# Performance work log

Hardware: AMD Instinct MI355X
Metric: run time of the kernel (lower is better)

## Reference

```python
import jax, jax.numpy as jnp
import numpy as np

N_NODES = 50000
N_EDGES = 800000
D = 128


def gcn_conv(x, W, b, src, dst, num_nodes):
    """PyG GCNConv: x @ W, add self-loops, symmetric normalization, scatter-add, + bias."""
    x = x @ W  # [N, out]
    loop = jnp.arange(num_nodes, dtype=src.dtype)
    s = jnp.concatenate([src, loop])  # [E+N]
    d = jnp.concatenate([dst, loop])
    w = jnp.ones(s.shape[0], x.dtype)  # edge_weight=None -> ones (self-loop fill=1)
    deg = jax.ops.segment_sum(w, d, num_segments=num_nodes)  # [N]
    dinv = jnp.where(deg > 0, jax.lax.rsqrt(deg), 0.0)
    norm = dinv[s] * dinv[d]  # [E+N]
    out = jax.ops.segment_sum(x[s] * norm[:, None], d, num_segments=num_nodes)
    return out + b


def setup_inputs() -> dict:
    key = jax.random.key(0)
    ks = jax.random.split(key, 8)
    sc = 1.0 / np.sqrt(D)
    x = jax.random.normal(ks[0], (N_NODES, D), dtype=jnp.float32)
    edge_index = jax.random.randint(ks[1], (2, N_EDGES), 0, N_NODES)
    W1 = jax.random.normal(ks[2], (D, D), dtype=jnp.float32) * sc
    W2 = jax.random.normal(ks[3], (D, D), dtype=jnp.float32) * sc
    W3 = jax.random.normal(ks[4], (D, D), dtype=jnp.float32) * sc
    b1 = jnp.zeros((D,), jnp.float32)
    b2 = jnp.zeros((D,), jnp.float32)
    b3 = jnp.zeros((D,), jnp.float32)
    return {"x": x, "edge_index": edge_index, "W1": W1, "b1": b1,
            "W2": W2, "b2": b2, "W3": W3, "b3": b3}


def reference(x, edge_index, W1, b1, W2, b2, W3, b3):
    src, dst = edge_index[0], edge_index[1]
    n = x.shape[0]
    x = jax.nn.relu(gcn_conv(x, W1, b1, src, dst, n))
    x = jax.nn.relu(gcn_conv(x, W2, b2, src, dst, n))
    return gcn_conv(x, W3, b3, src, dst, n)
```

## Files before the change

kernel.cpp:

```cpp
#include <hip/hip_runtime.h>
#include <hip/hip_fp16.h>
#include <math.h>

#define D 128

typedef __attribute__((ext_vector_type(8))) _Float16 half8;
typedef __attribute__((ext_vector_type(4))) float f32x4;



__global__ void prep_kernel(const float* __restrict__ W1, const float* __restrict__ W2,
                            const float* __restrict__ W3, __half* __restrict__ WhT,
                            int* __restrict__ cnt, int N) {
    int i = blockIdx.x * blockDim.x + threadIdx.x;
    if (i < 3 * D * D) {
        int l = i >> 14;
        int j = i & 16383;
        int n = j >> 7, k = j & 127;
        const float* W = (l == 0) ? W1 : (l == 1) ? W2 : W3;
        WhT[(size_t)i] = __float2half(W[(size_t)k * D + n]);
    }
    if (i < N) cnt[i] = 0;
}


__global__ void count_rank_kernel(const int* __restrict__ dst, int* __restrict__ cnt,
                                  int* __restrict__ rank, int E) {
    int e0 = (blockIdx.x * blockDim.x + threadIdx.x) * 8;
    if (e0 + 7 < E) {
        int4 da = *(const int4*)(dst + e0);
        int4 db = *(const int4*)(dst + e0 + 4);
        int4 ra, rb;
        ra.x = atomicAdd(&cnt[da.x], 1);
        ra.y = atomicAdd(&cnt[da.y], 1);
        ra.z = atomicAdd(&cnt[da.z], 1);
        ra.w = atomicAdd(&cnt[da.w], 1);
        rb.x = atomicAdd(&cnt[db.x], 1);
        rb.y = atomicAdd(&cnt[db.y], 1);
        rb.z = atomicAdd(&cnt[db.z], 1);
        rb.w = atomicAdd(&cnt[db.w], 1);
        *(int4*)(rank + e0)     = ra;
        *(int4*)(rank + e0 + 4) = rb;
    } else {
        for (int e = e0; e < E; ++e) rank[e] = atomicAdd(&cnt[dst[e]], 1);
    }
}

__global__ __launch_bounds__(1024) void scan_kernel(const int* __restrict__ cnt,
                                                    int* __restrict__ rowptr,
                                                    float* __restrict__ dinv,
                                                    int N) {
    __shared__ int wsum[16];
    int tid  = threadIdx.x;
    int lane = tid & 63;
    int wid  = tid >> 6;
    int C = ((N + 4095) / 4096) * 4;
    int start = tid * C;
    int end   = start + C; if (end > N) end = N;

    int local = 0;
    int i = start;
    for (; i + 3 < end; i += 4) {
        int4 v = *(const int4*)(cnt + i);
        local += v.x + v.y + v.z + v.w;
    }
    for (; i < end; ++i) local += cnt[i];

    int sc = local;
    #pragma unroll
    for (int off = 1; off < 64; off <<= 1) {
        int t = __shfl_up(sc, off, 64);
        if (lane >= off) sc += t;
    }
    if (lane == 63) wsum[wid] = sc;
    __syncthreads();
    if (tid < 16) {
        int w = wsum[tid];
        #pragma unroll
        for (int off = 1; off < 16; off <<= 1) {
            int t = __shfl_up(w, off, 16);
            if (tid >= off) w += t;
        }
        wsum[tid] = w;
    }
    __syncthreads();
    int run = ((wid > 0) ? wsum[wid - 1] : 0) + (sc - local);

    i = start;
    for (; i + 3 < end; i += 4) {
        int4 v = *(const int4*)(cnt + i);
        int4 rp;
        rp.x = run;
        rp.y = rp.x + v.x;
        rp.z = rp.y + v.y;
        rp.w = rp.z + v.z;
        run  = rp.w + v.w;
        *(int4*)(rowptr + i) = rp;
        float4 dv;
        dv.x = rsqrtf((float)v.x + 1.0f);
        dv.y = rsqrtf((float)v.y + 1.0f);
        dv.z = rsqrtf((float)v.z + 1.0f);
        dv.w = rsqrtf((float)v.w + 1.0f);
        *(float4*)(dinv + i) = dv;
    }
    for (; i < end; ++i) {
        int v = cnt[i];
        rowptr[i] = run; run += v;
        dinv[i] = rsqrtf((float)v + 1.0f);
    }
    if (tid == 0) rowptr[N] = wsum[15];
}


__global__ __launch_bounds__(256) void fill_gemm1_kernel(
    const int* __restrict__ src, const int* __restrict__ dst,
    const int* __restrict__ rank, const int* __restrict__ rowptr,
    int* __restrict__ col, int E, int fill_blocks,
    const float* __restrict__ X, const __half* __restrict__ WhT,
    const float* __restrict__ dinv, __half* __restrict__ Y, int M) {
    int tid = threadIdx.x;
    if ((int)blockIdx.x < fill_blocks) {
        int e0 = (blockIdx.x * 256 + tid) * 8;
        if (e0 + 7 < E) {
            int4 da = *(const int4*)(dst + e0);
            int4 db = *(const int4*)(dst + e0 + 4);
            int4 ra = *(const int4*)(rank + e0);
            int4 rb = *(const int4*)(rank + e0 + 4);
            int4 sa = *(const int4*)(src + e0);
            int4 sb = *(const int4*)(src + e0 + 4);
            int p0 = rowptr[da.x] + ra.x;
            int p1 = rowptr[da.y] + ra.y;
            int p2 = rowptr[da.z] + ra.z;
            int p3 = rowptr[da.w] + ra.w;
            int p4 = rowptr[db.x] + rb.x;
            int p5 = rowptr[db.y] + rb.y;
            int p6 = rowptr[db.z] + rb.z;
            int p7 = rowptr[db.w] + rb.w;
            col[p0] = sa.x; col[p1] = sa.y; col[p2] = sa.z; col[p3] = sa.w;
            col[p4] = sb.x; col[p5] = sb.y; col[p6] = sb.z; col[p7] = sb.w;
        } else {
            for (int e = e0; e < E; ++e) col[rowptr[dst[e]] + rank[e]] = src[e];
        }
        return;
    }
    int bid  = blockIdx.x - fill_blocks;
    int wave = tid >> 6;
    int lane = tid & 63;
    int quad = lane >> 4;
    int l16  = lane & 15;
    int m0   = bid * 64 + wave * 16;
    if (m0 >= M) return;

    f32x4 acc[8];
    #pragma unroll
    for (int t = 0; t < 8; ++t) acc[t] = (f32x4)0.0f;

    const float* xrow = X + (size_t)(m0 + l16) * D;

    #pragma unroll
    for (int ks = 0; ks < 4; ++ks) {
        int k0 = ks * 32 + quad * 8;
        float4 x0 = *(const float4*)(xrow + k0);
        float4 x1 = *(const float4*)(xrow + k0 + 4);
        half8 a;
        a[0] = (_Float16)x0.x; a[1] = (_Float16)x0.y;
        a[2] = (_Float16)x0.z; a[3] = (_Float16)x0.w;
        a[4] = (_Float16)x1.x; a[5] = (_Float16)x1.y;
        a[6] = (_Float16)x1.z; a[7] = (_Float16)x1.w;
        #pragma unroll
        for (int t = 0; t < 8; ++t) {
            half8 b = *(const half8*)(WhT + (size_t)(t * 16 + l16) * D + k0);
            acc[t] = __builtin_amdgcn_mfma_f32_16x16x32_f16(a, b, acc[t], 0, 0, 0);
        }
    }

    float4 dv = *(const float4*)(dinv + m0 + quad * 4);
    float dvs[4] = {dv.x, dv.y, dv.z, dv.w};
    #pragma unroll
    for (int t = 0; t < 8; ++t) {
        #pragma unroll
        for (int r = 0; r < 4; ++r) {
            int grow = m0 + quad * 4 + r;
            Y[((size_t)t * M + grow) * 16 + l16] = __float2half(acc[t][r] * dvs[r]);
        }
    }
}


__global__ __launch_bounds__(256) void gemm_s_kernel(const __half* __restrict__ Xs,
                                                     const __half* __restrict__ WhT,
                                                     const float* __restrict__ dinv,
                                                     __half* __restrict__ Ys, int M) {
    int tid  = threadIdx.x;
    int wave = tid >> 6;
    int lane = tid & 63;
    int quad = lane >> 4;
    int l16  = lane & 15;
    int m0   = blockIdx.x * 64 + wave * 16;
    if (m0 >= M) return;

    f32x4 acc[8];
    #pragma unroll
    for (int t = 0; t < 8; ++t) acc[t] = (f32x4)0.0f;

    int arow = m0 + l16;

    #pragma unroll
    for (int ks = 0; ks < 4; ++ks) {
        int k0 = ks * 32 + quad * 8;
        half8 a = *(const half8*)(Xs + ((size_t)(k0 >> 4) * M + arow) * 16 + (k0 & 15));
        #pragma unroll
        for (int t = 0; t < 8; ++t) {
            half8 b = *(const half8*)(WhT + (size_t)(t * 16 + l16) * D + k0);
            acc[t] = __builtin_amdgcn_mfma_f32_16x16x32_f16(a, b, acc[t], 0, 0, 0);
        }
    }

    float4 dv = *(const float4*)(dinv + m0 + quad * 4);
    float dvs[4] = {dv.x, dv.y, dv.z, dv.w};
    #pragma unroll
    for (int t = 0; t < 8; ++t) {
        #pragma unroll
        for (int r = 0; r < 4; ++r) {
            int grow = m0 + quad * 4 + r;
            Ys[((size_t)t * M + grow) * 16 + l16] = __float2half(acc[t][r] * dvs[r]);
        }
    }
}


template <bool FINAL>
__global__ __launch_bounds__(256) void agg_slice_kernel(
    const __half* __restrict__ ysIn, const int* __restrict__ rowptr,
    const int* __restrict__ col, const float* __restrict__ dinv,
    const float* __restrict__ bias, __half* __restrict__ outh,
    float* __restrict__ outf, int M) {
    int bid   = blockIdx.x;
    int slice = bid & 7;
    int chunk = bid >> 3;
    int tid  = threadIdx.x;
    int wave = tid >> 6;
    int lane = tid & 63;
    int g    = lane >> 3;
    int l8   = lane & 7;
    int row  = chunk * 32 + wave * 8 + g;
    bool valid = row < M;
    int c = valid ? row : M - 1;

    const __half* base = ysIn + (size_t)slice * M * 16;
    int s = rowptr[c], e = rowptr[c + 1];

    float2 bb = ((const float2*)bias)[slice * 8 + l8];

    __half2 hself = *(const __half2*)(base + (size_t)c * 16 + l8 * 2);
    float a0x = __low2float(hself), a0y = __high2float(hself);
    float a1x = 0.f, a1y = 0.f, a2x = 0.f, a2y = 0.f, a3x = 0.f, a3y = 0.f;

    int j = s;
    for (; j + 8 <= e; j += 8) {
        int c0 = col[j + 0], c1 = col[j + 1], c2 = col[j + 2], c3 = col[j + 3];
        int c4 = col[j + 4], c5 = col[j + 5], c6 = col[j + 6], c7 = col[j + 7];
        __half2 v0 = *(const __half2*)(base + (size_t)c0 * 16 + l8 * 2);
        __half2 v1 = *(const __half2*)(base + (size_t)c1 * 16 + l8 * 2);
        __half2 v2 = *(const __half2*)(base + (size_t)c2 * 16 + l8 * 2);
        __half2 v3 = *(const __half2*)(base + (size_t)c3 * 16 + l8 * 2);
        __half2 v4 = *(const __half2*)(base + (size_t)c4 * 16 + l8 * 2);
        __half2 v5 = *(const __half2*)(base + (size_t)c5 * 16 + l8 * 2);
        __half2 v6 = *(const __half2*)(base + (size_t)c6 * 16 + l8 * 2);
        __half2 v7 = *(const __half2*)(base + (size_t)c7 * 16 + l8 * 2);
        a0x += __low2float(v0); a0y += __high2float(v0);
        a1x += __low2float(v1); a1y += __high2float(v1);
        a2x += __low2float(v2); a2y += __high2float(v2);
        a3x += __low2float(v3); a3y += __high2float(v3);
        a0x += __low2float(v4); a0y += __high2float(v4);
        a1x += __low2float(v5); a1y += __high2float(v5);
        a2x += __low2float(v6); a2y += __high2float(v6);
        a3x += __low2float(v7); a3y += __high2float(v7);
    }
    for (; j + 4 <= e; j += 4) {
        int c0 = col[j + 0], c1 = col[j + 1], c2 = col[j + 2], c3 = col[j + 3];
        __half2 v0 = *(const __half2*)(base + (size_t)c0 * 16 + l8 * 2);
        __half2 v1 = *(const __half2*)(base + (size_t)c1 * 16 + l8 * 2);
        __half2 v2 = *(const __half2*)(base + (size_t)c2 * 16 + l8 * 2);
        __half2 v3 = *(const __half2*)(base + (size_t)c3 * 16 + l8 * 2);
        a0x += __low2float(v0); a0y += __high2float(v0);
        a1x += __low2float(v1); a1y += __high2float(v1);
        a2x += __low2float(v2); a2y += __high2float(v2);
        a3x += __low2float(v3); a3y += __high2float(v3);
    }
    for (; j < e; ++j) {
        int c0 = col[j];
        __half2 v0 = *(const __half2*)(base + (size_t)c0 * 16 + l8 * 2);
        a0x += __low2float(v0); a0y += __high2float(v0);
    }
    a0x += a1x + a2x + a3x;
    a0y += a1y + a2y + a3y;

    float dv = dinv[c];
    float rx = bb.x + dv * a0x;
    float ry = bb.y + dv * a0y;
    if (valid) {
        if (FINAL) {
            *(float2*)(outf + (size_t)row * D + slice * 16 + l8 * 2) = make_float2(rx, ry);
        } else {
            __half2 hv = __floats2half2_rn(fmaxf(rx, 0.f), fmaxf(ry, 0.f));
            *(__half2*)(outh + ((size_t)slice * M + row) * 16 + l8 * 2) = hv;
        }
    }
}


extern "C" void kernel_launch(void* const* d_in, const int* in_sizes, int n_in,
                              void* d_out, int out_size, void* d_ws, size_t ws_size,
                              hipStream_t stream) {
    const float* x   = (const float*)d_in[0];
    const int*   ei  = (const int*)d_in[1];
    const float* W1  = (const float*)d_in[2];
    const float* b1  = (const float*)d_in[3];
    const float* W2  = (const float*)d_in[4];
    const float* b2  = (const float*)d_in[5];
    const float* W3  = (const float*)d_in[6];
    const float* b3  = (const float*)d_in[7];
    float* out = (float*)d_out;

    const int N = in_sizes[0] / D;
    const int E = in_sizes[1] / 2;
    const int* src = ei;
    const int* dst = ei + E;

    char* ws = (char*)d_ws;
    size_t off = 0;
    auto alloc = [&](size_t bytes) {
        void* p = ws + off;
        off = (off + bytes + 255) & ~(size_t)255;
        return p;
    };
    __half* ys    = (__half*)alloc((size_t)N * D * sizeof(__half));
    __half* hs    = (__half*)alloc((size_t)N * D * sizeof(__half));
    int*   cnt    = (int*)alloc((size_t)N * sizeof(int));
    int*   rowptr = (int*)alloc((size_t)(N + 1) * sizeof(int));
    float* dinv   = (float*)alloc((size_t)N * sizeof(float));
    int*   rank   = (int*)alloc((size_t)E * sizeof(int));
    int*   col    = (int*)alloc((size_t)E * sizeof(int));
    __half* WhT   = (__half*)alloc((size_t)3 * D * D * sizeof(__half));
    (void)ws_size; (void)n_in; (void)out_size;

    int prep_threads = (3 * D * D > N) ? 3 * D * D : N;
    prep_kernel<<<(prep_threads + 255) / 256, 256, 0, stream>>>(W1, W2, W3, WhT, cnt, N);

    const int egrid = ((E + 7) / 8 + 255) / 256;
    count_rank_kernel<<<egrid, 256, 0, stream>>>(dst, cnt, rank, E);
    scan_kernel<<<1, 1024, 0, stream>>>(cnt, rowptr, dinv, N);

    const int gemm_grid = (N + 63) / 64;
    fill_gemm1_kernel<<<egrid + gemm_grid, 256, 0, stream>>>(
        src, dst, rank, rowptr, col, E, egrid, x, WhT, dinv, ys, N);

    const int nchunk = (N + 31) / 32;
    const int agg_grid = nchunk * 8;
    agg_slice_kernel<false><<<agg_grid, 256, 0, stream>>>(ys, rowptr, col, dinv, b1, hs, nullptr, N);
    gemm_s_kernel<<<gemm_grid, 256, 0, stream>>>(hs, WhT + 16384, dinv, ys, N);
    agg_slice_kernel<false><<<agg_grid, 256, 0, stream>>>(ys, rowptr, col, dinv, b2, hs, nullptr, N);
    gemm_s_kernel<<<gemm_grid, 256, 0, stream>>>(hs, WhT + 32768, dinv, ys, N);
    agg_slice_kernel<true><<<agg_grid, 256, 0, stream>>>(ys, rowptr, col, dinv, b3, nullptr, out, N);
}
```

Before: 345.2 us.

## Widen feature slices from 16 to 32 halves for aggregation gathers

Changes the sliced intermediate feature layout from 8 slices of 16 halves to 4 slices of 32 halves, updating the GEMM stores and loads to match. The aggregation kernel now uses 16 lanes per row, gathering 64-byte rows per neighbour and processing two row groups per block. This makes each random gather use more of every fetched cache line and halves the repeated passes over the CSR column indices. Per-block work rises and the layout-dependent indexing must stay consistent across all kernels.

Result: no change. 338.9 us (-1.8%).

```diff
diff --git a/kernel.cpp b/kernel.cpp
--- a/kernel.cpp
+++ b/kernel.cpp
@@ -181,7 +181,8 @@
         #pragma unroll
         for (int r = 0; r < 4; ++r) {
             int grow = m0 + quad * 4 + r;
-            Y[((size_t)t * M + grow) * 16 + l16] = __float2half(acc[t][r] * dvs[r]);
+            Y[((size_t)(t >> 1) * M + grow) * 32 + (t & 1) * 16 + l16] =
+                __float2half(acc[t][r] * dvs[r]);
         }
     }
 }
@@ -208,7 +209,7 @@
     #pragma unroll
     for (int ks = 0; ks < 4; ++ks) {
         int k0 = ks * 32 + quad * 8;
-        half8 a = *(const half8*)(Xs + ((size_t)(k0 >> 4) * M + arow) * 16 + (k0 & 15));
+        half8 a = *(const half8*)(Xs + ((size_t)ks * M + arow) * 32 + quad * 8);
         #pragma unroll
         for (int t = 0; t < 8; ++t) {
             half8 b = *(const half8*)(WhT + (size_t)(t * 16 + l16) * D + k0);
@@ -223,88 +224,94 @@
         #pragma unroll
         for (int r = 0; r < 4; ++r) {
             int grow = m0 + quad * 4 + r;
-            Ys[((size_t)t * M + grow) * 16 + l16] = __float2half(acc[t][r] * dvs[r]);
+            Ys[((size_t)(t >> 1) * M + grow) * 32 + (t & 1) * 16 + l16] =
+                __float2half(acc[t][r] * dvs[r]);
         }
     }
 }
 
 
 template <bool FINAL>
-__global__ __launch_bounds__(256) void agg_slice_kernel(
+__global__ __launch_bounds__(256) void agg_slice4_kernel(
     const __half* __restrict__ ysIn, const int* __restrict__ rowptr,
     const int* __restrict__ col, const float* __restrict__ dinv,
     const float* __restrict__ bias, __half* __restrict__ outh,
     float* __restrict__ outf, int M) {
     int bid   = blockIdx.x;
-    int slice = bid & 7;
+    int slice = bid & 3;
+    int sub   = (bid >> 2) & 1;
     int chunk = bid >> 3;
+    int row0  = (chunk * 2 + sub) * 32;
     int tid  = threadIdx.x;
     int wave = tid >> 6;
     int lane = tid & 63;
-    int g    = lane >> 3;
-    int l8   = lane & 7;
-    int row  = chunk * 32 + wave * 8 + g;
-    bool valid = row < M;
-    int c = valid ? row : M - 1;
-
-    const __half* base = ysIn + (size_t)slice * M * 16;
-    int s = rowptr[c], e = rowptr[c + 1];
-
-    float2 bb = ((const float2*)bias)[slice * 8 + l8];
-
-    __half2 hself = *(const __half2*)(base + (size_t)c * 16 + l8 * 2);
-    float a0x = __low2float(hself), a0y = __high2float(hself);
-    float a1x = 0.f, a1y = 0.f, a2x = 0.f, a2y = 0.f, a3x = 0.f, a3y = 0.f;
-
-    int j = s;
-    for (; j + 8 <= e; j += 8) {
-        int c0 = col[j + 0], c1 = col[j + 1], c2 = col[j + 2], c3 = col[j + 3];
-        int c4 = col[j + 4], c5 = col[j + 5], c6 = col[j + 6], c7 = col[j + 7];
-        __half2 v0 = *(const __half2*)(base + (size_t)c0 * 16 + l8 * 2);
-        __half2 v1 = *(const __half2*)(base + (size_t)c1 * 16 + l8 * 2);
-        __half2 v2 = *(const __half2*)(base + (size_t)c2 * 16 + l8 * 2);
-        __half2 v3 = *(const __half2*)(base + (size_t)c3 * 16 + l8 * 2);
-        __half2 v4 = *(const __half2*)(base + (size_t)c4 * 16 + l8 * 2);
-        __half2 v5 = *(const __half2*)(base + (size_t)c5 * 16 + l8 * 2);
-        __half2 v6 = *(const __half2*)(base + (size_t)c6 * 16 + l8 * 2);
-        __half2 v7 = *(const __half2*)(base + (size_t)c7 * 16 + l8 * 2);
-        a0x += __low2float(v0); a0y += __high2float(v0);
-        a1x += __low2float(v1); a1y += __high2float(v1);
-        a2x += __low2float(v2); a2y += __high2float(v2);
-        a3x += __low2float(v3); a3y += __high2float(v3);
-        a0x += __low2float(v4); a0y += __high2float(v4);
-        a1x += __low2float(v5); a1y += __high2float(v5);
-        a2x += __low2float(v6); a2y += __high2float(v6);
-        a3x += __low2float(v7); a3y += __high2float(v7);
-    }
-    for (; j + 4 <= e; j += 4) {
-        int c0 = col[j + 0], c1 = col[j + 1], c2 = col[j + 2], c3 = col[j + 3];
-        __half2 v0 = *(const __half2*)(base + (size_t)c0 * 16 + l8 * 2);
-        __half2 v1 = *(const __half2*)(base + (size_t)c1 * 16 + l8 * 2);
-        __half2 v2 = *(const __half2*)(base + (size_t)c2 * 16 + l8 * 2);
-        __half2 v3 = *(const __half2*)(base + (size_t)c3 * 16 + l8 * 2);
-        a0x += __low2float(v0); a0y += __high2float(v0);
-        a1x += __low2float(v1); a1y += __high2float(v1);
-        a2x += __low2float(v2); a2y += __high2float(v2);
-        a3x += __low2float(v3); a3y += __high2float(v3);
-    }
-    for (; j < e; ++j) {
-        int c0 = col[j];
-        __half2 v0 = *(const __half2*)(base + (size_t)c0 * 16 + l8 * 2);
-        a0x += __low2float(v0); a0y += __high2float(v0);
-    }
-    a0x += a1x + a2x + a3x;
-    a0y += a1y + a2y + a3y;
-
-    float dv = dinv[c];
-    float rx = bb.x + dv * a0x;
-    float ry = bb.y + dv * a0y;
-    if (valid) {
-        if (FINAL) {
-            *(float2*)(outf + (size_t)row * D + slice * 16 + l8 * 2) = make_float2(rx, ry);
-        } else {
-            __half2 hv = __floats2half2_rn(fmaxf(rx, 0.f), fmaxf(ry, 0.f));
-            *(__half2*)(outh + ((size_t)slice * M + row) * 16 + l8 * 2) = hv;
+    int g    = lane >> 4;
+    int l16  = lane & 15;
+
+    const __half* base = ysIn + (size_t)slice * M * 32;
+    float2 bb = ((const float2*)bias)[slice * 16 + l16];
+
+    #pragma unroll
+    for (int t = 0; t < 2; ++t) {
+        int row = row0 + t * 16 + wave * 4 + g;
+        bool valid = row < M;
+        int c = valid ? row : M - 1;
+        int s = rowptr[c], e = rowptr[c + 1];
+
+        __half2 hself = *(const __half2*)(base + (size_t)c * 32 + l16 * 2);
+        float a0x = __low2float(hself), a0y = __high2float(hself);
+        float a1x = 0.f, a1y = 0.f, a2x = 0.f, a2y = 0.f, a3x = 0.f, a3y = 0.f;
+
+        int j = s;
+        for (; j + 8 <= e; j += 8) {
+            int c0 = col[j + 0], c1 = col[j + 1], c2 = col[j + 2], c3 = col[j + 3];
+            int c4 = col[j + 4], c5 = col[j + 5], c6 = col[j + 6], c7 = col[j + 7];
+            __half2 v0 = *(const __half2*)(base + (size_t)c0 * 32 + l16 * 2);
+            __half2 v1 = *(const __half2*)(base + (size_t)c1 * 32 + l16 * 2);
+            __half2 v2 = *(const __half2*)(base + (size_t)c2 * 32 + l16 * 2);
+            __half2 v3 = *(const __half2*)(base + (size_t)c3 * 32 + l16 * 2);
+            __half2 v4 = *(const __half2*)(base + (size_t)c4 * 32 + l16 * 2);
+            __half2 v5 = *(const __half2*)(base + (size_t)c5 * 32 + l16 * 2);
+            __half2 v6 = *(const __half2*)(base + (size_t)c6 * 32 + l16 * 2);
+            __half2 v7 = *(const __half2*)(base + (size_t)c7 * 32 + l16 * 2);
+            a0x += __low2float(v0); a0y += __high2float(v0);
+            a1x += __low2float(v1); a1y += __high2float(v1);
+            a2x += __low2float(v2); a2y += __high2float(v2);
+            a3x += __low2float(v3); a3y += __high2float(v3);
+            a0x += __low2float(v4); a0y += __high2float(v4);
+            a1x += __low2float(v5); a1y += __high2float(v5);
+            a2x += __low2float(v6); a2y += __high2float(v6);
+            a3x += __low2float(v7); a3y += __high2float(v7);
+        }
+        for (; j + 4 <= e; j += 4) {
+            int c0 = col[j + 0], c1 = col[j + 1], c2 = col[j + 2], c3 = col[j + 3];
+            __half2 v0 = *(const __half2*)(base + (size_t)c0 * 32 + l16 * 2);
+            __half2 v1 = *(const __half2*)(base + (size_t)c1 * 32 + l16 * 2);
+            __half2 v2 = *(const __half2*)(base + (size_t)c2 * 32 + l16 * 2);
+            __half2 v3 = *(const __half2*)(base + (size_t)c3 * 32 + l16 * 2);
+            a0x += __low2float(v0); a0y += __high2float(v0);
+            a1x += __low2float(v1); a1y += __high2float(v1);
+            a2x += __low2float(v2); a2y += __high2float(v2);
+            a3x += __low2float(v3); a3y += __high2float(v3);
+        }
+        for (; j < e; ++j) {
+            int c0 = col[j];
+            __half2 v0 = *(const __half2*)(base + (size_t)c0 * 32 + l16 * 2);
+            a0x += __low2float(v0); a0y += __high2float(v0);
+        }
+        a0x += a1x + a2x + a3x;
+        a0y += a1y + a2y + a3y;
+
+        float dv = dinv[c];
+        float rx = bb.x + dv * a0x;
+        float ry = bb.y + dv * a0y;
+        if (valid) {
+            if (FINAL) {
+                *(float2*)(outf + (size_t)row * D + slice * 32 + l16 * 2) = make_float2(rx, ry);
+            } else {
+                __half2 hv = __floats2half2_rn(fmaxf(rx, 0.f), fmaxf(ry, 0.f));
+                *(__half2*)(outh + ((size_t)slice * M + row) * 32 + l16 * 2) = hv;
+            }
         }
     }
 }
@@ -356,11 +363,12 @@
     fill_gemm1_kernel<<<egrid + gemm_grid, 256, 0, stream>>>(
         src, dst, rank, rowptr, col, E, egrid, x, WhT, dinv, ys, N);
 
-    const int nchunk = (N + 31) / 32;
+    const int rows32 = (N + 31) / 32;
+    const int nchunk = (rows32 + 1) / 2;
     const int agg_grid = nchunk * 8;
-    agg_slice_kernel<false><<<agg_grid, 256, 0, stream>>>(ys, rowptr, col, dinv, b1, hs, nullptr, N);
+    agg_slice4_kernel<false><<<agg_grid, 256, 0, stream>>>(ys, rowptr, col, dinv, b1, hs, nullptr, N);
     gemm_s_kernel<<<gemm_grid, 256, 0, stream>>>(hs, WhT + 16384, dinv, ys, N);
-    agg_slice_kernel<false><<<agg_grid, 256, 0, stream>>>(ys, rowptr, col, dinv, b2, hs, nullptr, N);
+    agg_slice4_kernel<false><<<agg_grid, 256, 0, stream>>>(ys, rowptr, col, dinv, b2, hs, nullptr, N);
     gemm_s_kernel<<<gemm_grid, 256, 0, stream>>>(hs, WhT + 32768, dinv, ys, N);
-    agg_slice_kernel<true><<<agg_grid, 256, 0, stream>>>(ys, rowptr, col, dinv, b3, nullptr, out, N);
-}
+    agg_slice4_kernel<true><<<agg_grid, 256, 0, stream>>>(ys, rowptr, col, dinv, b3, nullptr, out, N);
+}
```
